# Kernel tuning notes

Measured on AMD Instinct MI355X. Metric: run time of the kernel, lower is better.

## Reference

```python
import jax, jax.numpy as jnp
import numpy as np

B, M, N, D, NH, DH = 2, 2048, 2048, 1024, 16, 64
STD = 0.02

def setup_inputs() -> dict:
    key = jax.random.key(0)
    ks = jax.random.split(key, 7)
    query = jax.random.normal(ks[0], (B, M, D), dtype=jnp.float32)
    key_value = jax.random.normal(ks[1], (B, N, D), dtype=jnp.float32)
    key_padding_mask = jax.random.uniform(ks[2], (B, N)) < 0.1
    # torch Linear weight is (out,in); store as (in,out) for x @ W
    W_Q = STD * jax.random.truncated_normal(ks[3], -2.0, 2.0, (D, NH * DH), dtype=jnp.float32)
    W_K = STD * jax.random.truncated_normal(ks[4], -2.0, 2.0, (D, NH * DH), dtype=jnp.float32)
    W_V = STD * jax.random.truncated_normal(ks[5], -2.0, 2.0, (D, NH * DH), dtype=jnp.float32)
    W_O = STD * jax.random.truncated_normal(ks[6], -2.0, 2.0, (NH * DH, D), dtype=jnp.float32)
    return {"query": query, "key_value": key_value, "key_padding_mask": key_padding_mask,
            "W_Q": W_Q, "W_K": W_K, "W_V": W_V, "W_O": W_O}

def reference(query, key_value, key_padding_mask, W_Q, W_K, W_V, W_O):
    scale = 1.0 / jnp.sqrt(jnp.float32(DH))
    Q = (query @ W_Q).reshape(B, M, NH, DH)       # (B,M,H,dh)
    K = (key_value @ W_K).reshape(B, N, NH, DH)   # (B,N,H,dh)
    V = (key_value @ W_V).reshape(B, N, NH, DH)
    scores = jnp.einsum('bmhd,bnhd->bhmn', Q, K) * scale  # (B,H,M,N)
    scores = jnp.where(key_padding_mask[:, None, None, :], -jnp.inf, scores)
    attn = jax.nn.softmax(scores, axis=-1)
    out = jnp.einsum('bhmn,bnhd->bmhd', attn, V).reshape(B, M, NH * DH)
    return out @ W_O
```

## Files before the change

### kernel.cpp

```cpp
#include <hip/hip_runtime.h>
#include <math.h>

#define BB 2
#define SEQ 2048
#define DMODEL 1024
#define NHH 16
#define DHH 64

typedef __bf16 bf16;
typedef __attribute__((ext_vector_type(8))) __bf16 bf16x8;
typedef __attribute__((ext_vector_type(4))) float f32x4;
typedef __attribute__((ext_vector_type(16))) float f32x16;

#define C1f 0.18033688011112042f
#define C2f -5.770780163555854f

__device__ __forceinline__ uint32_t cvtpk_bf16(float lo, float hi) {
  uint32_t r;
  asm("v_cvt_pk_bf16_f32 %0, %1, %2" : "=v"(r) : "v"(lo), "v"(hi));
  return r;
}
__device__ __forceinline__ void pl32swap(uint32_t& a, uint32_t& b) {
  asm("v_permlane32_swap_b32 %0, %1" : "+v"(a), "+v"(b));
}

__device__ __forceinline__ void gl_lds16(const bf16* g, bf16* l) {
  __builtin_amdgcn_global_load_lds(
      (const __attribute__((address_space(1))) void*)g,
      (__attribute__((address_space(3))) void*)l, 16, 0, 0);
}

__global__ __launch_bounds__(256) void prep(const float* __restrict__ query,
                                            const float* __restrict__ key_value,
                                            bf16* __restrict__ qbf,
                                            bf16* __restrict__ kvbf,
                                            const float* __restrict__ W0, const float* __restrict__ W1,
                                            const float* __restrict__ W2, const float* __restrict__ W3,
                                            bf16* __restrict__ O0, bf16* __restrict__ O1,
                                            bf16* __restrict__ O2, bf16* __restrict__ O3) {
  __shared__ bf16 T[64][72];
  const int bid = blockIdx.x;
  const int t = threadIdx.x;
  if (bid >= 1024) {
    const int bidc = bid - 1024;
    const float* in = (bidc >> 11) ? key_value : query;
    bf16* out = (bidc >> 11) ? kvbf : qbf;
    const int i = (bidc & 2047) * 256 + t;
    const float4* p = (const float4*)in + 2 * (size_t)i;
    float4 a = p[0], b = p[1];
    bf16x8 v;
    v[0] = (bf16)a.x; v[1] = (bf16)a.y; v[2] = (bf16)a.z; v[3] = (bf16)a.w;
    v[4] = (bf16)b.x; v[5] = (bf16)b.y; v[6] = (bf16)b.z; v[7] = (bf16)b.w;
    *((bf16x8*)out + i) = v;
    return;
  }
  const float* W; bf16* O;
  switch (bid >> 8) {
    case 0: W = W0; O = O0; break;
    case 1: W = W1; O = O1; break;
    case 2: W = W2; O = O2; break;
    default: W = W3; O = O3; break;
  }
  const int n0 = (bid & 15) * 64, k0 = ((bid >> 4) & 15) * 64;
  {
    int k = t >> 2, ns = (t & 3) * 16;
    const float* g = W + (size_t)(k0 + k) * DMODEL + n0 + ns;
#pragma unroll
    for (int q = 0; q < 4; ++q) {
      float4 f = *(const float4*)(g + 4 * q);
      T[ns + 4 * q + 0][k] = (bf16)f.x;
      T[ns + 4 * q + 1][k] = (bf16)f.y;
      T[ns + 4 * q + 2][k] = (bf16)f.z;
      T[ns + 4 * q + 3][k] = (bf16)f.w;
    }
  }
  __syncthreads();
  {
    int n = t >> 2, ks = (t & 3) * 16;
    bf16x8 a = *(const bf16x8*)&T[n][ks];
    bf16x8 b = *(const bf16x8*)&T[n][ks + 8];
    bf16* o = O + (size_t)(n0 + n) * DMODEL + k0 + ks;
    *(bf16x8*)o = a;
    *(bf16x8*)(o + 8) = b;
  }
}

template <bool F32OUT, int NT>
__device__ __forceinline__ void gemm128_body(const bf16* __restrict__ A,
                                             const bf16* __restrict__ Bt,
                                             float* __restrict__ Cf,
                                             bf16* __restrict__ Cb,
                                             bf16* As0, bf16* Bs0,
                                             bf16* As1, bf16* Bs1) {
  const int t = threadIdx.x;
  const int lane = t & 63, wave = t >> 6;
  const int l15 = lane & 15, quad = lane >> 4;
  const int bm = blockIdx.y * 128, bn = blockIdx.x * (32 * NT);
  const int wr = wave >> 1, wc = wave & 1;

  const int sr8 = lane >> 3;
  const int sc = lane & 7;
  const int ca = sc ^ (sr8 & 7);
  const bf16* gA = A + (size_t)(bm + wave * 32 + sr8) * DMODEL + ca * 8;
  const bf16* gB = Bt + (size_t)(bn + wave * (8 * NT) + sr8) * DMODEL + ca * 8;
  const int loA = wave * 32 * 64;
  const int loB = wave * (8 * NT) * 64;

  f32x4 acc[4][NT] = {};

#define STAGE(KT, AS, BS)                                                 \
  {                                                                       \
    const int kk = (KT) * 64;                                             \
    _Pragma("unroll") for (int j = 0; j < 4; ++j)                         \
        gl_lds16(gA + (size_t)(j * 8) * DMODEL + kk, (AS) + loA + j * 512); \
    _Pragma("unroll") for (int j = 0; j < NT; ++j)                        \
        gl_lds16(gB + (size_t)(j * 8) * DMODEL + kk, (BS) + loB + j * 512); \
  }

#define COMPUTE(AS, BS)                                                \
  {                                                                    \
    _Pragma("unroll") for (int ks = 0; ks < 2; ++ks) {                 \
      bf16x8 af[4], bfr[NT];                                           \
      _Pragma("unroll") for (int mt = 0; mt < 4; ++mt) {               \
        int row = wr * 64 + mt * 16 + l15;                             \
        int s = (ks * 4 + quad) ^ (row & 7);                           \
        af[mt] = *(const bf16x8*)&(AS)[row * 64 + s * 8];              \
      }                                                                \
      _Pragma("unroll") for (int nt = 0; nt < NT; ++nt) {              \
        int row = wc * (16 * NT) + nt * 16 + l15;                      \
        int s = (ks * 4 + quad) ^ (row & 7);                           \
        bfr[nt] = *(const bf16x8*)&(BS)[row * 64 + s * 8];             \
      }                                                                \
      _Pragma("unroll") for (int mt = 0; mt < 4; ++mt)                 \
          _Pragma("unroll") for (int nt = 0; nt < NT; ++nt)            \
              acc[mt][nt] = __builtin_amdgcn_mfma_f32_16x16x32_bf16(   \
                  af[mt], bfr[nt], acc[mt][nt], 0, 0, 0);              \
    }                                                                  \
  }

  STAGE(0, As0, Bs0);
  __syncthreads();

  for (int kt = 0; kt < DMODEL / 64; kt += 2) {
    if (kt + 1 < DMODEL / 64) STAGE(kt + 1, As1, Bs1);
    COMPUTE(As0, Bs0);
    __syncthreads();
    if (kt + 2 < DMODEL / 64) STAGE(kt + 2, As0, Bs0);
    COMPUTE(As1, Bs1);
    __syncthreads();
  }
#undef STAGE
#undef COMPUTE

#pragma unroll
  for (int mt = 0; mt < 4; ++mt)
#pragma unroll
    for (int nt = 0; nt < NT; ++nt)
#pragma unroll
      for (int r = 0; r < 4; ++r) {
        int row = bm + wr * 64 + mt * 16 + quad * 4 + r;
        int col = bn + wc * (16 * NT) + nt * 16 + l15;
        if (F32OUT) Cf[(size_t)row * DMODEL + col] = acc[mt][nt][r];
        else Cb[(size_t)row * DMODEL + col] = (bf16)acc[mt][nt][r];
      }
}

__global__ __launch_bounds__(256, 2) void gemm_qkv(const bf16* __restrict__ qbf,
                                                   const bf16* __restrict__ kvbf,
                                                   const bf16* __restrict__ WtQ,
                                                   const bf16* __restrict__ WtK,
                                                   const bf16* __restrict__ WtV,
                                                   bf16* __restrict__ Qb,
                                                   bf16* __restrict__ Kb,
                                                   bf16* __restrict__ Vb) {
  __shared__ bf16 As0[128 * 64], Bs0[128 * 64];
  __shared__ bf16 As1[128 * 64], Bs1[128 * 64];
  const bf16 *A, *Bt; bf16* C;
  switch (blockIdx.z) {
    case 0: A = qbf; Bt = WtQ; C = Qb; break;
    case 1: A = kvbf; Bt = WtK; C = Kb; break;
    default: A = kvbf; Bt = WtV; C = Vb; break;
  }
  gemm128_body<false, 4>(A, Bt, nullptr, C, As0, Bs0, As1, Bs1);
}

__global__ __launch_bounds__(256, 3) void gemm_out(const bf16* __restrict__ A,
                                                   const bf16* __restrict__ Wt,
                                                   float* __restrict__ C) {
  __shared__ bf16 As0[128 * 64], Bs0[64 * 64];
  __shared__ bf16 As1[128 * 64], Bs1[64 * 64];
  gemm128_body<true, 2>(A, Wt, C, nullptr, As0, Bs0, As1, Bs1);
}

__global__ __launch_bounds__(512, 4) void attn_mfma(const bf16* __restrict__ Qb,
                                                    const bf16* __restrict__ Kb,
                                                    const bf16* __restrict__ Vb,
                                                    const int* __restrict__ maskp,
                                                    bf16* __restrict__ Ob) {
  __shared__ bf16 Ks[2][2][64][68];
  __shared__ bf16 Vt[2][2][64][68];

  const int blk = blockIdx.x;
  const int h = blk & 15;
  const int b = (blk >> 4) & 1;
  const int qb = blk >> 5;
  const int t = threadIdx.x;
  const int wave = t >> 6, lane = t & 63;
  const int grp = wave >> 2;
  const int w4 = wave & 3;
  const int l31 = lane & 31, hi = lane >> 5;
  const int tl = t & 255;

  const int kr = tl >> 2, kq = tl & 3;
  const bf16* gK = Kb + (size_t)(b * SEQ + grp * 1024 + kr) * DMODEL + h * 64 + kq * 16;
  const int nv = (tl & 31) * 2, dc = (tl >> 5) * 8;
  const bf16* gV = Vb + (size_t)(b * SEQ + grp * 1024 + nv) * DMODEL + h * 64 + dc;
  const int* gM = maskp + b * SEQ + grp * 1024;

  {
    bf16x8 k0 = *(const bf16x8*)(gK);
    bf16x8 k1 = *(const bf16x8*)(gK + 8);
    *(bf16x8*)&Ks[grp][0][kr][kq * 16] = k0;
    *(bf16x8*)&Ks[grp][0][kr][kq * 16 + 8] = k1;
    bf16x8 v0 = *(const bf16x8*)(gV);
    bf16x8 v1 = *(const bf16x8*)(gV + DMODEL);
    union U { bf16x8 v; uint32_t dw[4]; } a, c;
    a.v = v0; c.v = v1;
#pragma unroll
    for (int d2 = 0; d2 < 4; ++d2) {
      *(uint32_t*)&Vt[grp][0][dc + 2 * d2 + 0][nv] = __builtin_amdgcn_perm(c.dw[d2], a.dw[d2], 0x05040100u);
      *(uint32_t*)&Vt[grp][0][dc + 2 * d2 + 1][nv] = __builtin_amdgcn_perm(c.dw[d2], a.dw[d2], 0x07060302u);
    }
  }
  int mcur = gM[lane];

  bf16x8 qf[4];
#pragma unroll
  for (int ks = 0; ks < 4; ++ks) {
    const bf16* g = Qb + (size_t)(b * SEQ + qb * 128 + w4 * 32 + l31) * DMODEL +
                    h * 64 + ks * 16 + hi * 8;
    qf[ks] = *(const bf16x8*)g;
  }

  f32x16 o0 = {}, o1 = {};
  float lsum = 0.f;

  __syncthreads();

  for (int it = 0; it < 16; ++it) {
    const int p = it & 1;
    const bool more = (it + 1) < 16;

    bf16x8 kreg0, kreg1, vreg0, vreg1;
    int mnext = 0;
    if (more) {
      const int nn = (it + 1) * 64;
      const bf16* gK2 = gK + (size_t)nn * DMODEL;
      const bf16* gV2 = gV + (size_t)nn * DMODEL;
      kreg0 = *(const bf16x8*)(gK2);
      kreg1 = *(const bf16x8*)(gK2 + 8);
      vreg0 = *(const bf16x8*)(gV2);
      vreg1 = *(const bf16x8*)(gV2 + DMODEL);
      mnext = gM[nn + lane];
    }

    f32x16 s0v = {}, s1v = {};
#pragma unroll
    for (int ks = 0; ks < 4; ++ks) {
      const int c = (ks * 2 + hi) * 8;
      bf16x8 ka0 = *(const bf16x8*)&Ks[grp][p][l31][c];
      bf16x8 ka1 = *(const bf16x8*)&Ks[grp][p][32 + l31][c];
      s0v = __builtin_amdgcn_mfma_f32_32x32x16_bf16(ka0, qf[ks], s0v, 0, 0, 0);
      s1v = __builtin_amdgcn_mfma_f32_32x32x16_bf16(ka1, qf[ks], s1v, 0, 0, 0);
    }

    const unsigned long long mb = __ballot(mcur == 0);

#pragma unroll
    for (int kt = 0; kt < 2; ++kt) {
      const f32x16 sv = kt ? s1v : s0v;
      const uint32_t ml = (uint32_t)(mb >> (kt * 32 + 4 * hi));
      float pm[16];
#pragma unroll
      for (int r = 0; r < 16; ++r) {
        const int bitc = (r & 3) + 8 * (r >> 2);
        float pex = __builtin_amdgcn_exp2f(sv[r] * C1f + C2f);
        pm[r] = ((ml >> bitc) & 1u) ? pex : 0.f;
        lsum += pm[r];
      }
      uint32_t w01 = cvtpk_bf16(pm[0], pm[1]),  w23 = cvtpk_bf16(pm[2], pm[3]);
      uint32_t w45 = cvtpk_bf16(pm[4], pm[5]),  w67 = cvtpk_bf16(pm[6], pm[7]);
      uint32_t w89 = cvtpk_bf16(pm[8], pm[9]),  wab = cvtpk_bf16(pm[10], pm[11]);
      uint32_t wcd = cvtpk_bf16(pm[12], pm[13]), wef = cvtpk_bf16(pm[14], pm[15]);
      pl32swap(w01, w45);
      pl32swap(w23, w67);
      pl32swap(w89, wcd);
      pl32swap(wab, wef);
      union BF { uint32_t u[4]; bf16x8 v; } f0, f1;
      f0.u[0] = w01; f0.u[1] = w23; f0.u[2] = w45; f0.u[3] = w67;
      f1.u[0] = w89; f1.u[1] = wab; f1.u[2] = wcd; f1.u[3] = wef;
      {
        bf16x8 va00 = *(const bf16x8*)&Vt[grp][p][0 + l31][(kt * 2 + 0) * 16 + hi * 8];
        bf16x8 va01 = *(const bf16x8*)&Vt[grp][p][0 + l31][(kt * 2 + 1) * 16 + hi * 8];
        o0 = __builtin_amdgcn_mfma_f32_32x32x16_bf16(va00, f0.v, o0, 0, 0, 0);
        o0 = __builtin_amdgcn_mfma_f32_32x32x16_bf16(va01, f1.v, o0, 0, 0, 0);
        bf16x8 va10 = *(const bf16x8*)&Vt[grp][p][32 + l31][(kt * 2 + 0) * 16 + hi * 8];
        bf16x8 va11 = *(const bf16x8*)&Vt[grp][p][32 + l31][(kt * 2 + 1) * 16 + hi * 8];
        o1 = __builtin_amdgcn_mfma_f32_32x32x16_bf16(va10, f0.v, o1, 0, 0, 0);
        o1 = __builtin_amdgcn_mfma_f32_32x32x16_bf16(va11, f1.v, o1, 0, 0, 0);
      }
    }

    if (more) {
      const int q = 1 - p;
      *(bf16x8*)&Ks[grp][q][kr][kq * 16] = kreg0;
      *(bf16x8*)&Ks[grp][q][kr][kq * 16 + 8] = kreg1;
      union U { bf16x8 v; uint32_t dw[4]; } a, c;
      a.v = vreg0; c.v = vreg1;
#pragma unroll
      for (int d2 = 0; d2 < 4; ++d2) {
        *(uint32_t*)&Vt[grp][q][dc + 2 * d2 + 0][nv] = __builtin_amdgcn_perm(c.dw[d2], a.dw[d2], 0x05040100u);
        *(uint32_t*)&Vt[grp][q][dc + 2 * d2 + 1][nv] = __builtin_amdgcn_perm(c.dw[d2], a.dw[d2], 0x07060302u);
      }
    }
    mcur = mnext;
    __syncthreads();
  }

  const float ltp = lsum + __shfl_xor(lsum, 32);

  float* sc = (float*)&Ks[0][0][0][0];
  float* scO = sc + 256;

  if (hi == 0) sc[wave * 32 + l31] = ltp;
  if (grp == 0) {
    float* dst = scO + ((size_t)(w4 * 64 + lane)) * 33;
#pragma unroll
    for (int r = 0; r < 16; ++r) {
      dst[r] = o0[r];
      dst[16 + r] = o1[r];
    }
  }
  __syncthreads();
  if (grp == 1) {
    const float ltot = sc[w4 * 32 + l31] + sc[(4 + w4) * 32 + l31];
    const float inv = 1.f / ltot;
    const float* src = scO + ((size_t)(w4 * 64 + lane)) * 33;
#pragma unroll
    for (int r = 0; r < 16; ++r) {
      o0[r] += src[r];
      o1[r] += src[16 + r];
    }
    bf16* gO = Ob + (size_t)(b * SEQ + qb * 128 + w4 * 32 + l31) * DMODEL + h * 64;
#pragma unroll
    for (int g = 0; g < 4; ++g) {
      uint2 st0, st1;
      st0.x = cvtpk_bf16(o0[4 * g + 0] * inv, o0[4 * g + 1] * inv);
      st0.y = cvtpk_bf16(o0[4 * g + 2] * inv, o0[4 * g + 3] * inv);
      st1.x = cvtpk_bf16(o1[4 * g + 0] * inv, o1[4 * g + 1] * inv);
      st1.y = cvtpk_bf16(o1[4 * g + 2] * inv, o1[4 * g + 3] * inv);
      *(uint2*)(gO + 8 * g + 4 * hi) = st0;
      *(uint2*)(gO + 32 + 8 * g + 4 * hi) = st1;
    }
  }
}

extern "C" void kernel_launch(void* const* d_in, const int* in_sizes, int n_in,
                              void* d_out, int out_size, void* d_ws, size_t ws_size,
                              hipStream_t stream) {
  (void)in_sizes; (void)n_in; (void)out_size; (void)ws_size;
  const float* query = (const float*)d_in[0];
  const float* key_value = (const float*)d_in[1];
  const int* mask = (const int*)d_in[2];
  const float* W_Q = (const float*)d_in[3];
  const float* W_K = (const float*)d_in[4];
  const float* W_V = (const float*)d_in[5];
  const float* W_O = (const float*)d_in[6];
  float* out = (float*)d_out;

  const size_t TOK = (size_t)BB * SEQ;
  const size_t TE = TOK * DMODEL;
  char* w = (char*)d_ws;
  bf16* qbf = (bf16*)w;   w += TE * 2;
  bf16* kvbf = (bf16*)w;  w += TE * 2;
  bf16* WtQ = (bf16*)w;   w += (size_t)DMODEL * DMODEL * 2;
  bf16* WtK = (bf16*)w;   w += (size_t)DMODEL * DMODEL * 2;
  bf16* WtV = (bf16*)w;   w += (size_t)DMODEL * DMODEL * 2;
  bf16* WtO = (bf16*)w;   w += (size_t)DMODEL * DMODEL * 2;
  bf16* Qbuf = (bf16*)w;  w += TE * 2;
  bf16* Kbuf = (bf16*)w;  w += TE * 2;
  bf16* Vbuf = (bf16*)w;  w += TE * 2;
  bf16* Obuf = (bf16*)w;  w += TE * 2;

  prep<<<5120, 256, 0, stream>>>(query, key_value, qbf, kvbf,
                                 W_Q, W_K, W_V, W_O, WtQ, WtK, WtV, WtO);

  gemm_qkv<<<dim3(DMODEL / 128, TOK / 128, 3), 256, 0, stream>>>(qbf, kvbf, WtQ, WtK, WtV,
                                                                 Qbuf, Kbuf, Vbuf);

  attn_mfma<<<BB * NHH * (SEQ / 128), 512, 0, stream>>>(Qbuf, Kbuf, Vbuf, mask, Obuf);

  gemm_out<<<dim3(DMODEL / 64, TOK / 128), 256, 0, stream>>>(Obuf, WtO, out);
}
```

Before: 202.7 us.

## Use 256x128 tiles with 512 threads for QKV projection GEMM

Rewrites the QKV projection GEMM as a standalone kernel with 256x128 output tiles, 8 waves and a single-buffered LDS stage, replacing the templated 128x128 double-buffered body. Larger tiles raise arithmetic intensity per global load and halve the block count. In exchange it drops the double-buffer overlap of global loads with MFMA compute, adds two barriers per k-step, and may reduce occupancy. The output GEMM is inlined with unchanged behaviour.

```diff
diff --git a/kernel.cpp b/kernel.cpp
--- a/kernel.cpp
+++ b/kernel.cpp
@@ -85,13 +85,90 @@
   }
 }
 
-template <bool F32OUT, int NT>
-__device__ __forceinline__ void gemm128_body(const bf16* __restrict__ A,
-                                             const bf16* __restrict__ Bt,
-                                             float* __restrict__ Cf,
-                                             bf16* __restrict__ Cb,
-                                             bf16* As0, bf16* Bs0,
-                                             bf16* As1, bf16* Bs1) {
+__global__ __launch_bounds__(512) void gemm_qkv(const bf16* __restrict__ qbf,
+                                                const bf16* __restrict__ kvbf,
+                                                const bf16* __restrict__ WtQ,
+                                                const bf16* __restrict__ WtK,
+                                                const bf16* __restrict__ WtV,
+                                                bf16* __restrict__ Qb,
+                                                bf16* __restrict__ Kb,
+                                                bf16* __restrict__ Vb) {
+  __shared__ bf16 As[256 * 64];
+  __shared__ bf16 Bs[128 * 64];
+  const bf16 *A, *Bt; bf16* C;
+  switch (blockIdx.z) {
+    case 0: A = qbf; Bt = WtQ; C = Qb; break;
+    case 1: A = kvbf; Bt = WtK; C = Kb; break;
+    default: A = kvbf; Bt = WtV; C = Vb; break;
+  }
+
+  const int t = threadIdx.x;
+  const int lane = t & 63, wave = t >> 6;
+  const int l15 = lane & 15, quad = lane >> 4;
+  const int bm = blockIdx.y * 256, bn = blockIdx.x * 128;
+  const int wr = wave >> 1, wc = wave & 1;
+
+  const int srow = t >> 3;
+  const int sc = t & 7;
+  const int ca = sc ^ (srow & 7);
+  const bf16* gA = A + (size_t)(bm + srow) * DMODEL + ca * 8;
+  const bf16* gB = Bt + (size_t)(bn + srow) * DMODEL + ca * 8;
+  const int lo = wave * 512;
+
+  f32x4 acc[4][4] = {};
+
+  for (int kt = 0; kt < DMODEL / 64; ++kt) {
+    const int kk = kt * 64;
+#pragma unroll
+    for (int j = 0; j < 4; ++j)
+      gl_lds16(gA + (size_t)(j * 64) * DMODEL + kk, As + lo + j * 4096);
+#pragma unroll
+    for (int j = 0; j < 2; ++j)
+      gl_lds16(gB + (size_t)(j * 64) * DMODEL + kk, Bs + lo + j * 4096);
+    __syncthreads();
+#pragma unroll
+    for (int ks = 0; ks < 2; ++ks) {
+      bf16x8 af[4], bfr[4];
+#pragma unroll
+      for (int mt = 0; mt < 4; ++mt) {
+        int row = wr * 64 + mt * 16 + l15;
+        int s = (ks * 4 + quad) ^ (row & 7);
+        af[mt] = *(const bf16x8*)&As[row * 64 + s * 8];
+      }
+#pragma unroll
+      for (int nt = 0; nt < 4; ++nt) {
+        int row = wc * 64 + nt * 16 + l15;
+        int s = (ks * 4 + quad) ^ (row & 7);
+        bfr[nt] = *(const bf16x8*)&Bs[row * 64 + s * 8];
+      }
+#pragma unroll
+      for (int mt = 0; mt < 4; ++mt)
+#pragma unroll
+        for (int nt = 0; nt < 4; ++nt)
+          acc[mt][nt] = __builtin_amdgcn_mfma_f32_16x16x32_bf16(af[mt], bfr[nt], acc[mt][nt], 0, 0, 0);
+    }
+    __syncthreads();
+  }
+
+#pragma unroll
+  for (int mt = 0; mt < 4; ++mt)
+#pragma unroll
+    for (int nt = 0; nt < 4; ++nt)
+#pragma unroll
+      for (int r = 0; r < 4; ++r) {
+        int row = bm + wr * 64 + mt * 16 + quad * 4 + r;
+        int col = bn + wc * 64 + nt * 16 + l15;
+        C[(size_t)row * DMODEL + col] = (bf16)acc[mt][nt][r];
+      }
+}
+
+__global__ __launch_bounds__(256, 3) void gemm_out(const bf16* __restrict__ A,
+                                                   const bf16* __restrict__ Wt,
+                                                   float* __restrict__ C) {
+  __shared__ bf16 As0[128 * 64], Bs0[64 * 64];
+  __shared__ bf16 As1[128 * 64], Bs1[64 * 64];
+  const int NT = 2;
+
   const int t = threadIdx.x;
   const int lane = t & 63, wave = t >> 6;
   const int l15 = lane & 15, quad = lane >> 4;
@@ -102,7 +179,7 @@
   const int sc = lane & 7;
   const int ca = sc ^ (sr8 & 7);
   const bf16* gA = A + (size_t)(bm + wave * 32 + sr8) * DMODEL + ca * 8;
-  const bf16* gB = Bt + (size_t)(bn + wave * (8 * NT) + sr8) * DMODEL + ca * 8;
+  const bf16* gB = Wt + (size_t)(bn + wave * (8 * NT) + sr8) * DMODEL + ca * 8;
   const int loA = wave * 32 * 64;
   const int loB = wave * (8 * NT) * 64;
 
@@ -160,36 +237,8 @@
       for (int r = 0; r < 4; ++r) {
         int row = bm + wr * 64 + mt * 16 + quad * 4 + r;
         int col = bn + wc * (16 * NT) + nt * 16 + l15;
-        if (F32OUT) Cf[(size_t)row * DMODEL + col] = acc[mt][nt][r];
-        else Cb[(size_t)row * DMODEL + col] = (bf16)acc[mt][nt][r];
-      }
-}
-
-__global__ __launch_bounds__(256, 2) void gemm_qkv(const bf16* __restrict__ qbf,
-                                                   const bf16* __restrict__ kvbf,
-                                                   const bf16* __restrict__ WtQ,
-                                                   const bf16* __restrict__ WtK,
-                                                   const bf16* __restrict__ WtV,
-                                                   bf16* __restrict__ Qb,
-                                                   bf16* __restrict__ Kb,
-                                                   bf16* __restrict__ Vb) {
-  __shared__ bf16 As0[128 * 64], Bs0[128 * 64];
-  __shared__ bf16 As1[128 * 64], Bs1[128 * 64];
-  const bf16 *A, *Bt; bf16* C;
-  switch (blockIdx.z) {
-    case 0: A = qbf; Bt = WtQ; C = Qb; break;
-    case 1: A = kvbf; Bt = WtK; C = Kb; break;
-    default: A = kvbf; Bt = WtV; C = Vb; break;
-  }
-  gemm128_body<false, 4>(A, Bt, nullptr, C, As0, Bs0, As1, Bs1);
-}
-
-__global__ __launch_bounds__(256, 3) void gemm_out(const bf16* __restrict__ A,
-                                                   const bf16* __restrict__ Wt,
-                                                   float* __restrict__ C) {
-  __shared__ bf16 As0[128 * 64], Bs0[64 * 64];
-  __shared__ bf16 As1[128 * 64], Bs1[64 * 64];
-  gemm128_body<true, 2>(A, Wt, C, nullptr, As0, Bs0, As1, Bs1);
+        C[(size_t)row * DMODEL + col] = acc[mt][nt][r];
+      }
 }
 
 __global__ __launch_bounds__(512, 4) void attn_mfma(const bf16* __restrict__ Qb,
@@ -395,7 +444,7 @@
   prep<<<5120, 256, 0, stream>>>(query, key_value, qbf, kvbf,
                                  W_Q, W_K, W_V, W_O, WtQ, WtK, WtV, WtO);
 
-  gemm_qkv<<<dim3(DMODEL / 128, TOK / 128, 3), 256, 0, stream>>>(qbf, kvbf, WtQ, WtK, WtV,
+  gemm_qkv<<<dim3(DMODEL / 128, TOK / 256, 3), 512, 0, stream>>>(qbf, kvbf, WtQ, WtK, WtV,
                                                                  Qbuf, Kbuf, Vbuf);
 
   attn_mfma<<<BB * NHH * (SEQ / 128), 512, 0, stream>>>(Qbuf, Kbuf, Vbuf, mask, Obuf);
```

After: 198.5 us. 2.0% less time.
